# Kernel optimization log

Measured on AMD Instinct MI355X. Metric: run time of the kernel, lower is better.

Reference implementation:

```python
import jax, jax.numpy as jnp
import numpy as np

SCALE = 2
STRIDE = 1


def setup_inputs() -> dict:
    key = jax.random.key(0)
    kx, kw, kb = jax.random.split(key, 3)
    B, Cin, H, W = 16, 128, 64, 64
    Cout, kh, kw_ = 128, 3, 3
    N = Cout * Cin * kh * kw_
    bound = 1.0 / np.sqrt(N)
    x = jax.random.normal(kx, (B, Cin, H, W), dtype=jnp.float32)
    weight = jax.random.uniform(kw, (Cout, Cin, kh, kw_), dtype=jnp.float32,
                                minval=-bound, maxval=bound)
    bias = jax.random.uniform(kb, (Cout,), dtype=jnp.float32,
                              minval=-bound, maxval=bound)
    return {"x": x, "weight": weight, "bias": bias}


def reference(x, weight, bias):
    # Nearest-neighbor upsample: each input pixel replicated SCALE x SCALE.
    up = jnp.repeat(jnp.repeat(x, SCALE, axis=2), SCALE, axis=3)  # [B,C,H*s,W*s]
    # Conv2d (cross-correlation, no padding), same math as unfold + matmul.
    out = jax.lax.conv_general_dilated(
        up, weight,
        window_strides=(STRIDE, STRIDE),
        padding="VALID",
        dimension_numbers=("NCHW", "OIHW", "NCHW"),
    )
    return out + bias[None, :, None, None]
```

## Files before the change

kernel.cpp:

```cpp
#include <hip/hip_runtime.h>
#include <hip/hip_bf16.h>
#include <stdint.h>


#define B_    16
#define CIN   128
#define HIN   64
#define WIN   64
#define COUT  128
#define HO    126
#define WO    126
#define M_TOT (B_ * 63 * 63)
#define BM    64
#define BK    32
#define KTILES 16
#define AS_STRIDE 40

typedef __bf16 bf16;
typedef __bf16 bf16x4 __attribute__((ext_vector_type(4)));
typedef __bf16 bf16x8 __attribute__((ext_vector_type(8)));
typedef float  floatx4 __attribute__((ext_vector_type(4)));

__global__ void prep_weights(const float* __restrict__ w, bf16* __restrict__ wb) {
    int idx = blockIdx.x * 256 + threadIdx.x;
    if (idx >= 4 * KTILES * COUT * BK) return;
    int k32 = idx & 31;
    int o   = (idx >> 5) & 127;
    int par = (idx >> 12) & 3;
    int kt  = idx >> 14;
    int k = kt * 32 + k32;
    int c = k >> 2, u = (k >> 1) & 1, v = k & 1;
    int a = par >> 1, bp = par & 1;
    int dy0, dy1, ndy, dx0, dx1, ndx;
    if (u == 0) { if (a == 0) { dy0 = 0; dy1 = 1; ndy = 2; } else { dy0 = 0; dy1 = 0; ndy = 1; } }
    else        { if (a == 0) { dy0 = 2; dy1 = 2; ndy = 1; } else { dy0 = 1; dy1 = 2; ndy = 2; } }
    if (v == 0) { if (bp == 0) { dx0 = 0; dx1 = 1; ndx = 2; } else { dx0 = 0; dx1 = 0; ndx = 1; } }
    else        { if (bp == 0) { dx0 = 2; dx1 = 2; ndx = 1; } else { dx0 = 1; dx1 = 2; ndx = 2; } }
    const float* wp = w + (o * CIN + c) * 9;
    float s = wp[dy0 * 3 + dx0];
    if (ndx == 2) s += wp[dy0 * 3 + dx1];
    if (ndy == 2) { s += wp[dy1 * 3 + dx0]; if (ndx == 2) s += wp[dy1 * 3 + dx1]; }
    wb[idx] = (bf16)s;
}

__global__ __launch_bounds__(512)
void upconv_gemm(const float* __restrict__ x, const bf16* __restrict__ wb,
                 const float* __restrict__ bias, float* __restrict__ out) {
    __shared__ bf16 As[BM * AS_STRIDE];
    __shared__ bf16 Bs[4 * COUT * BK];

    const int t    = threadIdx.x;
    const int lane = t & 63;
    const int wid  = t >> 6;
    const int a    = wid >> 2;
    const int oq   = wid & 3;
    const int quad = lane >> 4;
    const int l15  = lane & 15;
    const int kq   = quad * 8;

    const int m0 = blockIdx.x * BM;

    const int ml = t & 63;
    const int m_mine = m0 + ml;
    const bool mvalid = (m_mine < M_TOT);
    int b_ = 0, p_ = 0, q_ = 0;
    if (mvalid) { b_ = m_mine / 3969; int rr = m_mine - b_ * 3969; p_ = rr / 63; q_ = rr - p_ * 63; }
    const float* xbase = x + ((size_t)(b_ * CIN) * HIN + p_) * WIN + q_;

    floatx4 acc[2][4][2] = {};

    for (int kt = 0; kt < KTILES; ++kt) {
        __syncthreads();
        {
            const uint4* src = (const uint4*)(wb + (size_t)kt * (4 * COUT * BK));
            uint4* dst = (uint4*)Bs;
            #pragma unroll
            for (int i = 0; i < 4; ++i) dst[t + i * 512] = src[t + i * 512];
        }
        {
            const int c = kt * 8 + wid;
            float f00 = 0.f, f01 = 0.f, f10 = 0.f, f11 = 0.f;
            if (mvalid) {
                const float* pa = xbase + (size_t)c * (HIN * WIN);
                f00 = pa[0]; f01 = pa[1]; f10 = pa[WIN]; f11 = pa[WIN + 1];
            }
            bf16x4 v; v[0] = (bf16)f00; v[1] = (bf16)f01; v[2] = (bf16)f10; v[3] = (bf16)f11;
            *(bf16x4*)&As[ml * AS_STRIDE + wid * 4] = v;
        }
        __syncthreads();
        bf16x8 af[4], wf[2][2];
        #pragma unroll
        for (int i = 0; i < 4; ++i)
            af[i] = *(const bf16x8*)&As[(i * 16 + l15) * AS_STRIDE + kq];
        #pragma unroll
        for (int bp = 0; bp < 2; ++bp)
            #pragma unroll
            for (int nt = 0; nt < 2; ++nt)
                wf[bp][nt] = *(const bf16x8*)&Bs[(a * 2 + bp) * (COUT * BK)
                                                + (oq * 32 + nt * 16 + l15) * BK + kq];
        #pragma unroll
        for (int bp = 0; bp < 2; ++bp)
            #pragma unroll
            for (int mt = 0; mt < 4; ++mt)
                #pragma unroll
                for (int nt = 0; nt < 2; ++nt)
                    acc[bp][mt][nt] = __builtin_amdgcn_mfma_f32_16x16x32_bf16(
                        wf[bp][nt], af[mt], acc[bp][mt][nt], 0, 0, 0);
    }

    float bv[2][4];
    #pragma unroll
    for (int nt = 0; nt < 2; ++nt)
        #pragma unroll
        for (int ri = 0; ri < 4; ++ri)
            bv[nt][ri] = bias[oq * 32 + nt * 16 + quad * 4 + ri];

    #pragma unroll
    for (int mt = 0; mt < 4; ++mt) {
        const int m = m0 + mt * 16 + l15;
        const bool v = (m < M_TOT);
        int b = 0, p = 0, q = 0;
        if (v) { b = m / 3969; int rr = m - b * 3969; p = rr / 63; q = rr - p * 63; }
        float* base = out + (size_t)b * (COUT * HO * WO) + (size_t)(2 * p + a) * WO + 2 * q;
        #pragma unroll
        for (int nt = 0; nt < 2; ++nt) {
            #pragma unroll
            for (int ri = 0; ri < 4; ++ri) {
                const int o = oq * 32 + nt * 16 + quad * 4 + ri;
                if (v) {
                    float2 r = make_float2(acc[0][mt][nt][ri] + bv[nt][ri],
                                           acc[1][mt][nt][ri] + bv[nt][ri]);
                    *(float2*)(base + (size_t)o * (HO * WO)) = r;
                }
            }
        }
    }
}

extern "C" void kernel_launch(void* const* d_in, const int* in_sizes, int n_in,
                              void* d_out, int out_size, void* d_ws, size_t ws_size,
                              hipStream_t stream) {
    const float* x    = (const float*)d_in[0];
    const float* w    = (const float*)d_in[1];
    const float* bias = (const float*)d_in[2];
    float* out = (float*)d_out;
    bf16* wb = (bf16*)d_ws;

    prep_weights<<<(4 * KTILES * COUT * BK + 255) / 256, 256, 0, stream>>>(w, wb);

    dim3 grid((M_TOT + BM - 1) / BM);
    upconv_gemm<<<grid, 512, 0, stream>>>(x, wb, bias, out);
}
```

Before: 219.3 us.

## Stage full A tile in LDS once and read weights directly from global

The per-k-tile loop with two barriers is replaced by a single upfront load of the whole 64x512 input patch tile into shared memory, followed by one barrier. The weight tile is no longer staged through LDS; each wave reads its bf16 weight fragments directly from global memory, relying on the L1/L2 cache. The k loop is fully unrolled and launch bounds request 4 blocks per CU. This removes per-iteration synchronization and LDS weight copies, at the cost of uncoalesced, latency-exposed global weight loads and about 66KB of LDS per block, which limits how many blocks fit per CU.

```diff
diff --git a/kernel.cpp b/kernel.cpp
--- a/kernel.cpp
+++ b/kernel.cpp
@@ -12,9 +12,8 @@
 #define WO    126
 #define M_TOT (B_ * 63 * 63)
 #define BM    64
-#define BK    32
 #define KTILES 16
-#define AS_STRIDE 40
+#define AS_K  520
 
 typedef __bf16 bf16;
 typedef __bf16 bf16x4 __attribute__((ext_vector_type(4)));
@@ -23,7 +22,7 @@
 
 __global__ void prep_weights(const float* __restrict__ w, bf16* __restrict__ wb) {
     int idx = blockIdx.x * 256 + threadIdx.x;
-    if (idx >= 4 * KTILES * COUT * BK) return;
+    if (idx >= 4 * KTILES * COUT * 32) return;
     int k32 = idx & 31;
     int o   = (idx >> 5) & 127;
     int par = (idx >> 12) & 3;
@@ -43,11 +42,10 @@
     wb[idx] = (bf16)s;
 }
 
-__global__ __launch_bounds__(512)
+__global__ __launch_bounds__(512, 4)
 void upconv_gemm(const float* __restrict__ x, const bf16* __restrict__ wb,
                  const float* __restrict__ bias, float* __restrict__ out) {
-    __shared__ bf16 As[BM * AS_STRIDE];
-    __shared__ bf16 Bs[4 * COUT * BK];
+    __shared__ bf16 As[BM * AS_K];
 
     const int t    = threadIdx.x;
     const int lane = t & 63;
@@ -60,44 +58,42 @@
 
     const int m0 = blockIdx.x * BM;
 
-    const int ml = t & 63;
+    const int ml = lane;
     const int m_mine = m0 + ml;
     const bool mvalid = (m_mine < M_TOT);
     int b_ = 0, p_ = 0, q_ = 0;
     if (mvalid) { b_ = m_mine / 3969; int rr = m_mine - b_ * 3969; p_ = rr / 63; q_ = rr - p_ * 63; }
     const float* xbase = x + ((size_t)(b_ * CIN) * HIN + p_) * WIN + q_;
 
+    #pragma unroll
+    for (int cc = 0; cc < 16; ++cc) {
+        const int c = wid * 16 + cc;
+        float f00 = 0.f, f01 = 0.f, f10 = 0.f, f11 = 0.f;
+        if (mvalid) {
+            const float* pa = xbase + (size_t)c * (HIN * WIN);
+            f00 = pa[0]; f01 = pa[1]; f10 = pa[WIN]; f11 = pa[WIN + 1];
+        }
+        bf16x4 v; v[0] = (bf16)f00; v[1] = (bf16)f01; v[2] = (bf16)f10; v[3] = (bf16)f11;
+        *(bf16x4*)&As[ml * AS_K + c * 4] = v;
+    }
+    __syncthreads();
+
+    const bf16* wwave = wb + ((size_t)(a * 2) * COUT + oq * 32 + l15) * 32 + kq;
+
     floatx4 acc[2][4][2] = {};
 
+    #pragma unroll
     for (int kt = 0; kt < KTILES; ++kt) {
-        __syncthreads();
-        {
-            const uint4* src = (const uint4*)(wb + (size_t)kt * (4 * COUT * BK));
-            uint4* dst = (uint4*)Bs;
-            #pragma unroll
-            for (int i = 0; i < 4; ++i) dst[t + i * 512] = src[t + i * 512];
-        }
-        {
-            const int c = kt * 8 + wid;
-            float f00 = 0.f, f01 = 0.f, f10 = 0.f, f11 = 0.f;
-            if (mvalid) {
-                const float* pa = xbase + (size_t)c * (HIN * WIN);
-                f00 = pa[0]; f01 = pa[1]; f10 = pa[WIN]; f11 = pa[WIN + 1];
-            }
-            bf16x4 v; v[0] = (bf16)f00; v[1] = (bf16)f01; v[2] = (bf16)f10; v[3] = (bf16)f11;
-            *(bf16x4*)&As[ml * AS_STRIDE + wid * 4] = v;
-        }
-        __syncthreads();
         bf16x8 af[4], wf[2][2];
         #pragma unroll
         for (int i = 0; i < 4; ++i)
-            af[i] = *(const bf16x8*)&As[(i * 16 + l15) * AS_STRIDE + kq];
+            af[i] = *(const bf16x8*)&As[(i * 16 + l15) * AS_K + kt * 32 + kq];
         #pragma unroll
         for (int bp = 0; bp < 2; ++bp)
             #pragma unroll
             for (int nt = 0; nt < 2; ++nt)
-                wf[bp][nt] = *(const bf16x8*)&Bs[(a * 2 + bp) * (COUT * BK)
-                                                + (oq * 32 + nt * 16 + l15) * BK + kq];
+                wf[bp][nt] = *(const bf16x8*)(wwave
+                    + ((size_t)kt * 4 * COUT + (size_t)bp * COUT + nt * 16) * 32);
         #pragma unroll
         for (int bp = 0; bp < 2; ++bp)
             #pragma unroll
@@ -146,7 +142,7 @@
     float* out = (float*)d_out;
     bf16* wb = (bf16*)d_ws;
 
-    prep_weights<<<(4 * KTILES * COUT * BK + 255) / 256, 256, 0, stream>>>(w, wb);
+    prep_weights<<<(4 * KTILES * COUT * 32 + 255) / 256, 256, 0, stream>>>(w, wb);
 
     dim3 grid((M_TOT + BM - 1) / BM);
     upconv_gemm<<<grid, 512, 0, stream>>>(x, wb, bias, out);
```

Measured after the change: 217.2 us. About the same (-1.0%).
